# Optimization experiments

Measured on AMD Instinct MI355X. Metric: run time of the kernel, lower is better.

Reference implementation:

```python
import jax, jax.numpy as jnp
import numpy as np

DIM = 256
N_EMBED = 8192
DECAY = 0.1
COMMITMENT = 1.0
EPS = 1e-05


def setup_inputs() -> dict:
    key = jax.random.key(0)
    k1, k2, k3, k4 = jax.random.split(key, 4)
    return {
        "input": jax.random.normal(k1, (8, 1024, DIM), dtype=jnp.float32),
        "embed": jax.random.normal(k2, (DIM, N_EMBED), dtype=jnp.float32),
        "cluster_size": jax.random.uniform(k3, (N_EMBED,), dtype=jnp.float32),
        "embed_avg": jax.random.normal(k4, (DIM, N_EMBED), dtype=jnp.float32),
    }


def reference(input, embed, cluster_size, embed_avg):
    dtype = input.dtype
    flatten = input.reshape(-1, DIM)  # [N, dim]
    # squared euclidean distance to each code: [N, n_embed]
    dist = (
        jnp.sum(flatten * flatten, axis=1, keepdims=True)
        - 2.0 * (flatten @ embed)
        + jnp.sum(embed * embed, axis=0, keepdims=True)
    )
    embed_ind_flat = jnp.argmin(dist, axis=1)  # [N]
    embed_ind = embed_ind_flat.reshape(input.shape[:-1])
    quantize = jnp.take(embed.T, embed_ind, axis=0)  # [..., dim]

    # EMA codebook update (training path), via segment sums instead of dense one-hot
    bins = jax.ops.segment_sum(
        jnp.ones_like(embed_ind_flat, dtype=dtype), embed_ind_flat, num_segments=N_EMBED
    )  # one_hot.sum(0)
    embed_sum = jax.ops.segment_sum(flatten, embed_ind_flat, num_segments=N_EMBED).T  # [dim, n_embed]
    cluster_size_new = cluster_size * DECAY + (1.0 - DECAY) * bins
    embed_avg_new = embed_avg * DECAY + (1.0 - DECAY) * embed_sum
    smoothed = (cluster_size_new + EPS) / (jnp.sum(cluster_size_new) + N_EMBED * EPS)
    cs = smoothed * jnp.sum(cluster_size_new)
    embed_normalized = embed_avg_new / cs[None, :]

    commit_loss = jnp.mean((jax.lax.stop_gradient(quantize) - input) ** 2) * COMMITMENT
    quantize_st = input + jax.lax.stop_gradient(quantize - input)
    return (quantize_st, embed_ind, commit_loss, embed_normalized, cluster_size_new, embed_avg_new)
```

## Files before the change

kernel.cpp:

```cpp
#include <hip/hip_runtime.h>

typedef unsigned short u16;
typedef __attribute__((ext_vector_type(8))) short short8;
typedef __attribute__((ext_vector_type(4))) float f32x4;

#define DIM    256
#define NE     8192
#define NROWS  8192
#define DECAY  0.1f
#define EPS_F  1e-5f
#define CRANGES 16
#define CPAIRS  16
#define MQ      384u

#define OUT_Q    0
#define OUT_IND  2097152
#define OUT_LOSS 2105344
#define OUT_NORM 2105345
#define OUT_CSN  4202497
#define OUT_AVG  4210689

#define WS_CAND  65536
#define WS_ENORM 1114112
#define WS_BASEQ 1146880
#define WS_SUM   1179648
#define WS_BINS  9568256
#define WS_LOSS  9601024
#define WS_S     9601032
#define WS_XB    9601040
#define WS_ETB   13795344
#define WS_ET32  17989648
#define WS_ZLEN  (WS_XB - WS_SUM)

__device__ __forceinline__ unsigned f32_ord(float f)
{
    unsigned u = __float_as_uint(f);
    return (u & 0x80000000u) ? ~u : (u | 0x80000000u);
}
__device__ __forceinline__ u16 bf16rne(float f)
{
    unsigned u = __float_as_uint(f);
    return (u16)((u + 0x7fffu + ((u >> 16) & 1u)) >> 16);
}
__device__ __forceinline__ void gload16(const void* g, void* l)
{
    __builtin_amdgcn_global_load_lds((const __attribute__((address_space(1))) unsigned int*)g,
                                     (__attribute__((address_space(3))) unsigned int*)l, 16, 0, 0);
}

__global__ __launch_bounds__(256) void vq_cvt_x_k(const float* __restrict__ X, u16* __restrict__ Xb)
{
    const int i = blockIdx.x * 256 + threadIdx.x;
    const float4 a = ((const float4*)X)[i * 2];
    const float4 b = ((const float4*)X)[i * 2 + 1];
    short8 v;
    v[0] = (short)bf16rne(a.x); v[1] = (short)bf16rne(a.y);
    v[2] = (short)bf16rne(a.z); v[3] = (short)bf16rne(a.w);
    v[4] = (short)bf16rne(b.x); v[5] = (short)bf16rne(b.y);
    v[6] = (short)bf16rne(b.z); v[7] = (short)bf16rne(b.w);
    *(short8*)(Xb + (size_t)i * 8) = v;
}

__global__ __launch_bounds__(256) void vq_trans_e_k(const float* __restrict__ E,
                                                    float* __restrict__ ET32,
                                                    u16* __restrict__ ETb,
                                                    float* __restrict__ enorm,
                                                    float* __restrict__ baseq)
{
    __shared__ float T[64][65];
    const int t = threadIdx.x;
    const int j0 = blockIdx.x * 64;
    const int jc = t >> 2, seg = t & 3;
    const int j = j0 + jc;
    float esum = 0.f;

    for (int d0 = 0; d0 < DIM; d0 += 64) {
        if (d0) __syncthreads();
        #pragma unroll
        for (int p = 0; p < 4; ++p) {
            const int dr = p * 16 + (t >> 4);
            const float4 v = *(const float4*)(E + (size_t)(d0 + dr) * NE + j0 + (t & 15) * 4);
            T[dr][(t & 15) * 4 + 0] = v.x; T[dr][(t & 15) * 4 + 1] = v.y;
            T[dr][(t & 15) * 4 + 2] = v.z; T[dr][(t & 15) * 4 + 3] = v.w;
        }
        __syncthreads();
        float vals[16];
        #pragma unroll
        for (int i = 0; i < 16; ++i) vals[i] = T[seg * 16 + i][jc];
        float4* o32 = (float4*)(ET32 + (size_t)j * DIM + d0 + seg * 16);
        o32[0] = make_float4(vals[0], vals[1], vals[2], vals[3]);
        o32[1] = make_float4(vals[4], vals[5], vals[6], vals[7]);
        o32[2] = make_float4(vals[8], vals[9], vals[10], vals[11]);
        o32[3] = make_float4(vals[12], vals[13], vals[14], vals[15]);
        short8 b0, b1;
        #pragma unroll
        for (int i = 0; i < 8; ++i) { b0[i] = (short)bf16rne(vals[i]); b1[i] = (short)bf16rne(vals[8 + i]); }
        *(short8*)(ETb + (size_t)j * DIM + d0 + seg * 16) = b0;
        *(short8*)(ETb + (size_t)j * DIM + d0 + seg * 16 + 8) = b1;
        #pragma unroll
        for (int i = 0; i < 16; ++i) esum += vals[i] * vals[i];
    }
    esum += __shfl_xor(esum, 1, 4);
    esum += __shfl_xor(esum, 2, 4);
    if (seg == 0) {
        enorm[j] = esum;
        baseq[j] = (esum + 512.f) * 256.f;
    }
}

__global__ __launch_bounds__(256, 2) void vq_scan_k(const u16* __restrict__ Xb,
                                                    const u16* __restrict__ ETb,
                                                    const float* __restrict__ baseq,
                                                    unsigned* __restrict__ cand)
{
    __shared__ u16 Bs[2][16][512];

    const int tid = threadIdx.x;
    const int w = tid >> 6, l = tid & 63;
    const int lane16 = l & 15, g = l >> 4;
    const int rowbase = blockIdx.x * 256 + w * 64;
    const int c0 = blockIdx.y * 512;

    short8 af[4][8];
    #pragma unroll
    for (int sub = 0; sub < 4; ++sub)
        #pragma unroll
        for (int k8 = 0; k8 < 8; ++k8) {
            af[sub][k8] = *(const short8*)(Xb + (size_t)(rowbase + sub * 16 + lane16) * DIM + k8 * 32 + g * 8);
            asm volatile("" : "+a"(af[sub][k8]));
        }

    unsigned s0[16], s1[16];
    #pragma unroll
    for (int i = 0; i < 16; ++i) { s0[i] = 0xFFFFFFFFu; s1[i] = 0xFFFFFFFFu; }

    const u16* gsrc = ETb + (size_t)(c0 + lane16) * DIM + (size_t)w * 64 + g * 8;

    gload16(gsrc,                 &Bs[0][2 * w + 0][0]);
    gload16(gsrc + 32,            &Bs[0][2 * w + 1][0]);
    gload16(gsrc + 16 * DIM,      &Bs[0][8 + 2 * w + 0][0]);
    gload16(gsrc + 16 * DIM + 32, &Bs[0][8 + 2 * w + 1][0]);
    asm volatile("s_waitcnt vmcnt(0)" ::: "memory");
    __builtin_amdgcn_s_barrier();

    int buf = 0;
    #pragma unroll 1
    for (int p = 0; p < CPAIRS; ++p) {
        if (p + 1 < CPAIRS) {
            const u16* nsrc = gsrc + (size_t)(p + 1) * 32 * DIM;
            gload16(nsrc,                 &Bs[buf ^ 1][2 * w + 0][0]);
            gload16(nsrc + 32,            &Bs[buf ^ 1][2 * w + 1][0]);
            gload16(nsrc + 16 * DIM,      &Bs[buf ^ 1][8 + 2 * w + 0][0]);
            gload16(nsrc + 16 * DIM + 32, &Bs[buf ^ 1][8 + 2 * w + 1][0]);
        }
        #pragma unroll
        for (int half = 0; half < 2; ++half) {
            const int col = c0 + (p * 2 + half) * 16 + lane16;
            const float bq = baseq[col];
            f32x4 acc[4];
            #pragma unroll
            for (int sub = 0; sub < 4; ++sub) acc[sub] = {0.f, 0.f, 0.f, 0.f};
            #pragma unroll
            for (int k8 = 0; k8 < 8; ++k8) {
                const short8 bf = *(const short8*)&Bs[buf][half * 8 + k8][l * 8];
                #pragma unroll
                for (int sub = 0; sub < 4; ++sub)
                    acc[sub] = __builtin_amdgcn_mfma_f32_16x16x32_bf16(af[sub][k8], bf, acc[sub], 0, 0, 0);
            }
            #pragma unroll
            for (int sub = 0; sub < 4; ++sub)
                #pragma unroll
                for (int r = 0; r < 4; ++r) {
                    const int i = sub * 4 + r;
                    const float qf = fmaf(acc[sub][r], -512.f, bq);
                    const unsigned key = (((unsigned)qf) << 13) | (unsigned)col;
                    const unsigned t = max(s0[i], key);
                    s0[i] = min(s0[i], key);
                    s1[i] = min(s1[i], t);
                }
        }
        asm volatile("s_waitcnt vmcnt(0)" ::: "memory");
        __builtin_amdgcn_s_barrier();
        buf ^= 1;
    }

    #pragma unroll
    for (int m = 1; m < 16; m <<= 1) {
        #pragma unroll
        for (int i = 0; i < 16; ++i) {
            const unsigned o0 = __shfl_xor(s0[i], m);
            const unsigned o1 = __shfl_xor(s1[i], m);
            const unsigned t0 = min(s0[i], o0);
            const unsigned t1 = min(max(s0[i], o0), min(s1[i], o1));
            s0[i] = t0; s1[i] = t1;
        }
    }
    if (lane16 == 0) {
        #pragma unroll
        for (int i = 0; i < 16; ++i) {
            const int row = rowbase + (i >> 2) * 16 + g * 4 + (i & 3);
            cand[((size_t)row * CRANGES + blockIdx.y) * 2 + 0] = s0[i];
            cand[((size_t)row * CRANGES + blockIdx.y) * 2 + 1] = s1[i];
        }
    }
}

__global__ __launch_bounds__(256) void vq_finalize_k(const unsigned* __restrict__ cand,
                                                     const float* __restrict__ X,
                                                     const float* __restrict__ ET32,
                                                     const float* __restrict__ enorm,
                                                     float* __restrict__ out_q,
                                                     float* __restrict__ out_ind,
                                                     float* __restrict__ ws_sum,
                                                     float* __restrict__ bins,
                                                     double* __restrict__ loss)
{
    __shared__ int sj[4];
    const int tid = threadIdx.x;
    const int w = tid >> 6, l = tid & 63;
    const int row = blockIdx.x * 4 + w;

    unsigned key = 0xFFFFFFFFu;
    if (l < 32) key = cand[(size_t)row * 32 + l];
    unsigned qmin = key;
    #pragma unroll
    for (int m = 32; m; m >>= 1) qmin = min(qmin, __shfl_xor(qmin, m));
    const unsigned qthr = (qmin >> 13) + MQ;
    unsigned long long mask = __ballot((l < 32) && ((key >> 13) <= qthr));
    const float4 xv = *(const float4*)(X + (size_t)row * DIM + l * 4);
    unsigned long long best = 0xFFFFFFFFFFFFFFFFull;
    while (mask) {
        const int src = __builtin_ctzll(mask);
        mask &= mask - 1;
        const int col = (int)(__shfl(key, src) & 8191u);
        const float4 ev = *(const float4*)(ET32 + (size_t)col * DIM + l * 4);
        float s = xv.x * ev.x + xv.y * ev.y + xv.z * ev.z + xv.w * ev.w;
        #pragma unroll
        for (int m = 32; m; m >>= 1) s += __shfl_xor(s, m);
        const float d = enorm[col] - 2.f * s;
        const unsigned long long k64 = ((unsigned long long)f32_ord(d) << 32) | (unsigned)col;
        best = (k64 < best) ? k64 : best;
    }
    if (l == 0) {
        const int j = (int)(best & 8191u);
        sj[w] = j;
        out_ind[row] = (float)j;
    }
    __syncthreads();

    float lsum = 0.f;
    #pragma unroll
    for (int q = 0; q < 4; ++q) {
        const int r = blockIdx.x * 4 + q;
        const int j = sj[q];
        const float x  = X[(size_t)r * DIM + tid];
        const float qv = ET32[(size_t)j * DIM + tid];
        out_q[(size_t)r * DIM + tid] = x + (qv - x);
        const float d = qv - x;
        lsum += d * d;
        atomicAdd(&ws_sum[(size_t)j * DIM + tid], x);
        if (tid == 0) atomicAdd(&bins[j], 1.0f);
    }
    #pragma unroll
    for (int off = 32; off > 0; off >>= 1) lsum += __shfl_down(lsum, off);
    __shared__ double wred[4];
    if ((tid & 63) == 0) wred[tid >> 6] = (double)lsum;
    __syncthreads();
    if (tid == 0) atomicAdd(loss, wred[0] + wred[1] + wred[2] + wred[3]);
}

__global__ __launch_bounds__(256) void vq_csn_k(const float* __restrict__ cs,
                                                const float* __restrict__ bins,
                                                float* __restrict__ out_csn,
                                                float* __restrict__ out_loss,
                                                const double* __restrict__ loss,
                                                double* __restrict__ S)
{
    const int tid = threadIdx.x;
    const int i = blockIdx.x * 256 + tid;
    const float csn = cs[i] * DECAY + (1.0f - DECAY) * bins[i];
    out_csn[i] = csn;
    double v = (double)csn;
    #pragma unroll
    for (int off = 32; off > 0; off >>= 1) v += __shfl_down(v, off);
    __shared__ double wred[4];
    if ((tid & 63) == 0) wred[tid >> 6] = v;
    __syncthreads();
    if (tid == 0) atomicAdd(S, wred[0] + wred[1] + wred[2] + wred[3]);
    if (blockIdx.x == 0 && tid == 0) out_loss[0] = (float)(loss[0] * (1.0 / 2097152.0));
}

__global__ __launch_bounds__(256) void vq_embed_k(const float* __restrict__ EA,
                                                  const float* __restrict__ cs,
                                                  const float* __restrict__ bins,
                                                  const float* __restrict__ ws_sum,
                                                  const double* __restrict__ Sp,
                                                  float* __restrict__ out_norm,
                                                  float* __restrict__ out_avg)
{
    __shared__ float T[64][69];
    const int tid = threadIdx.x;
    const int j0 = blockIdx.x * 64;
    const int d0 = blockIdx.y * 64;
    #pragma unroll
    for (int p = 0; p < 4; ++p) {
        const int jr = (tid >> 4) + p * 16;
        const int dc = (tid & 15) * 4;
        const float4 v = *(const float4*)(ws_sum + (size_t)(j0 + jr) * DIM + d0 + dc);
        T[jr][dc + 0] = v.x; T[jr][dc + 1] = v.y; T[jr][dc + 2] = v.z; T[jr][dc + 3] = v.w;
    }
    __syncthreads();
    const double S = Sp[0];
    const float fac = (float)(S / (S + (double)NE * 1e-5));
    const int jc = tid & 63;
    const int j  = j0 + jc;
    const float csn  = cs[j] * DECAY + (1.0f - DECAY) * bins[j];
    const float cs_j = (csn + EPS_F) * fac;
    const int drb = (tid >> 6) * 16;
    #pragma unroll
    for (int p = 0; p < 16; ++p) {
        const int dr = drb + p;
        const float sum = T[jc][dr];
        const float ea  = EA[(size_t)(d0 + dr) * NE + j];
        const float ean = DECAY * ea + (1.0f - DECAY) * sum;
        out_avg[(size_t)(d0 + dr) * NE + j]  = ean;
        out_norm[(size_t)(d0 + dr) * NE + j] = ean / cs_j;
    }
}

extern "C" void kernel_launch(void* const* d_in, const int* in_sizes, int n_in,
                              void* d_out, int out_size, void* d_ws, size_t ws_size,
                              hipStream_t stream)
{
    const float* X  = (const float*)d_in[0];
    const float* E  = (const float*)d_in[1];
    const float* CS = (const float*)d_in[2];
    const float* EA = (const float*)d_in[3];
    float* out = (float*)d_out;
    char*  ws  = (char*)d_ws;

    unsigned* cand  = (unsigned*)(ws + WS_CAND);
    float*  enorm  = (float*)(ws + WS_ENORM);
    float*  baseq  = (float*)(ws + WS_BASEQ);
    float*  ws_sum = (float*)(ws + WS_SUM);
    float*  bins   = (float*)(ws + WS_BINS);
    double* loss   = (double*)(ws + WS_LOSS);
    double* S      = (double*)(ws + WS_S);
    u16*    Xb     = (u16*)(ws + WS_XB);
    u16*    ETb    = (u16*)(ws + WS_ETB);
    float*  ET32   = (float*)(ws + WS_ET32);

    hipMemsetAsync(ws + WS_SUM, 0, WS_ZLEN, stream);

    vq_cvt_x_k<<<1024, 256, 0, stream>>>(X, Xb);
    vq_trans_e_k<<<NE / 64, 256, 0, stream>>>(E, ET32, ETb, enorm, baseq);
    vq_scan_k<<<dim3(NROWS / 256, CRANGES), 256, 0, stream>>>(Xb, ETb, baseq, cand);
    vq_finalize_k<<<NROWS / 4, 256, 0, stream>>>(cand, X, ET32, enorm, out + OUT_Q, out + OUT_IND, ws_sum, bins, loss);
    vq_csn_k<<<NE / 256, 256, 0, stream>>>(CS, bins, out + OUT_CSN, out + OUT_LOSS, loss, S);
    vq_embed_k<<<dim3(NE / 64, DIM / 64), 256, 0, stream>>>(EA, CS, bins, ws_sum, S, out + OUT_NORM, out + OUT_AVG);
}
```

Measured before the change: 107.5 us.

## Merge prep kernels, fold csn into embed, widen scan tiles, add MFMA priority

Combines the X bf16 conversion and the codebook transpose into one prep kernel that also sums cluster_size. The later kernel that computed the new cluster sizes is removed. Its sum is instead derived algebraically from the cluster_size sum, since the bins always total the row count, and its output writes move into the embed kernel. This removes two launches and an atomic reduction. The scan kernel's LDS tile is doubled to stage 64 codes per iteration, halving barrier count, and s_setprio is raised around the MFMA block. The larger LDS footprint may lower occupancy.

New measurement: 103.5 us. -3.8%, faster.

```diff
diff --git a/kernel.cpp b/kernel.cpp
--- a/kernel.cpp
+++ b/kernel.cpp
@@ -10,7 +10,7 @@
 #define DECAY  0.1f
 #define EPS_F  1e-5f
 #define CRANGES 16
-#define CPAIRS  16
+#define CPH     8
 #define MQ      384u
 
 #define OUT_Q    0
@@ -26,7 +26,7 @@
 #define WS_SUM   1179648
 #define WS_BINS  9568256
 #define WS_LOSS  9601024
-#define WS_S     9601032
+#define WS_SCS   9601032
 #define WS_XB    9601040
 #define WS_ETB   13795344
 #define WS_ET32  17989648
@@ -48,63 +48,84 @@
                                      (__attribute__((address_space(3))) unsigned int*)l, 16, 0, 0);
 }
 
-__global__ __launch_bounds__(256) void vq_cvt_x_k(const float* __restrict__ X, u16* __restrict__ Xb)
-{
-    const int i = blockIdx.x * 256 + threadIdx.x;
-    const float4 a = ((const float4*)X)[i * 2];
-    const float4 b = ((const float4*)X)[i * 2 + 1];
-    short8 v;
-    v[0] = (short)bf16rne(a.x); v[1] = (short)bf16rne(a.y);
-    v[2] = (short)bf16rne(a.z); v[3] = (short)bf16rne(a.w);
-    v[4] = (short)bf16rne(b.x); v[5] = (short)bf16rne(b.y);
-    v[6] = (short)bf16rne(b.z); v[7] = (short)bf16rne(b.w);
-    *(short8*)(Xb + (size_t)i * 8) = v;
-}
-
-__global__ __launch_bounds__(256) void vq_trans_e_k(const float* __restrict__ E,
-                                                    float* __restrict__ ET32,
-                                                    u16* __restrict__ ETb,
-                                                    float* __restrict__ enorm,
-                                                    float* __restrict__ baseq)
-{
-    __shared__ float T[64][65];
+__global__ __launch_bounds__(256) void vq_prep_k(const float* __restrict__ X,
+                                                 const float* __restrict__ E,
+                                                 const float* __restrict__ CS,
+                                                 u16* __restrict__ Xb,
+                                                 float* __restrict__ ET32,
+                                                 u16* __restrict__ ETb,
+                                                 float* __restrict__ enorm,
+                                                 float* __restrict__ baseq,
+                                                 double* __restrict__ sumcs)
+{
+    const int bid = blockIdx.x;
     const int t = threadIdx.x;
-    const int j0 = blockIdx.x * 64;
-    const int jc = t >> 2, seg = t & 3;
-    const int j = j0 + jc;
-    float esum = 0.f;
-
-    for (int d0 = 0; d0 < DIM; d0 += 64) {
-        if (d0) __syncthreads();
-        #pragma unroll
-        for (int p = 0; p < 4; ++p) {
-            const int dr = p * 16 + (t >> 4);
-            const float4 v = *(const float4*)(E + (size_t)(d0 + dr) * NE + j0 + (t & 15) * 4);
-            T[dr][(t & 15) * 4 + 0] = v.x; T[dr][(t & 15) * 4 + 1] = v.y;
-            T[dr][(t & 15) * 4 + 2] = v.z; T[dr][(t & 15) * 4 + 3] = v.w;
-        }
+
+    if (bid < 128) {
+        __shared__ float T[64][65];
+        const int j0 = bid * 64;
+        const int jc = t >> 2, seg = t & 3;
+        const int j = j0 + jc;
+        float esum = 0.f;
+        for (int d0 = 0; d0 < DIM; d0 += 64) {
+            if (d0) __syncthreads();
+            #pragma unroll
+            for (int p = 0; p < 4; ++p) {
+                const int dr = p * 16 + (t >> 4);
+                const float4 v = *(const float4*)(E + (size_t)(d0 + dr) * NE + j0 + (t & 15) * 4);
+                T[dr][(t & 15) * 4 + 0] = v.x; T[dr][(t & 15) * 4 + 1] = v.y;
+                T[dr][(t & 15) * 4 + 2] = v.z; T[dr][(t & 15) * 4 + 3] = v.w;
+            }
+            __syncthreads();
+            float vals[16];
+            #pragma unroll
+            for (int i = 0; i < 16; ++i) vals[i] = T[seg * 16 + i][jc];
+            float4* o32 = (float4*)(ET32 + (size_t)j * DIM + d0 + seg * 16);
+            o32[0] = make_float4(vals[0], vals[1], vals[2], vals[3]);
+            o32[1] = make_float4(vals[4], vals[5], vals[6], vals[7]);
+            o32[2] = make_float4(vals[8], vals[9], vals[10], vals[11]);
+            o32[3] = make_float4(vals[12], vals[13], vals[14], vals[15]);
+            short8 b0, b1;
+            #pragma unroll
+            for (int i = 0; i < 8; ++i) { b0[i] = (short)bf16rne(vals[i]); b1[i] = (short)bf16rne(vals[8 + i]); }
+            *(short8*)(ETb + (size_t)j * DIM + d0 + seg * 16) = b0;
+            *(short8*)(ETb + (size_t)j * DIM + d0 + seg * 16 + 8) = b1;
+            #pragma unroll
+            for (int i = 0; i < 16; ++i) esum += vals[i] * vals[i];
+        }
+        esum += __shfl_xor(esum, 1, 4);
+        esum += __shfl_xor(esum, 2, 4);
+        if (seg == 0) {
+            enorm[j] = esum;
+            baseq[j] = (esum + 512.f) * 256.f;
+        }
+    } else if (bid < 256) {
+        const int chunk = bid - 128;
+        #pragma unroll
+        for (int it = 0; it < 8; ++it) {
+            const int gi = chunk * 2048 + it * 256 + t;
+            const float4 a = ((const float4*)X)[gi * 2];
+            const float4 b = ((const float4*)X)[gi * 2 + 1];
+            short8 v;
+            v[0] = (short)bf16rne(a.x); v[1] = (short)bf16rne(a.y);
+            v[2] = (short)bf16rne(a.z); v[3] = (short)bf16rne(a.w);
+            v[4] = (short)bf16rne(b.x); v[5] = (short)bf16rne(b.y);
+            v[6] = (short)bf16rne(b.z); v[7] = (short)bf16rne(b.w);
+            *(short8*)(Xb + (size_t)gi * 8) = v;
+        }
+    } else {
+        double s = 0.0;
+        #pragma unroll
+        for (int it = 0; it < 8; ++it) {
+            const float4 v = ((const float4*)CS)[it * 256 + t];
+            s += (double)v.x + (double)v.y + (double)v.z + (double)v.w;
+        }
+        #pragma unroll
+        for (int off = 32; off > 0; off >>= 1) s += __shfl_down(s, off);
+        __shared__ double wred[4];
+        if ((t & 63) == 0) wred[t >> 6] = s;
         __syncthreads();
-        float vals[16];
-        #pragma unroll
-        for (int i = 0; i < 16; ++i) vals[i] = T[seg * 16 + i][jc];
-        float4* o32 = (float4*)(ET32 + (size_t)j * DIM + d0 + seg * 16);
-        o32[0] = make_float4(vals[0], vals[1], vals[2], vals[3]);
-        o32[1] = make_float4(vals[4], vals[5], vals[6], vals[7]);
-        o32[2] = make_float4(vals[8], vals[9], vals[10], vals[11]);
-        o32[3] = make_float4(vals[12], vals[13], vals[14], vals[15]);
-        short8 b0, b1;
-        #pragma unroll
-        for (int i = 0; i < 8; ++i) { b0[i] = (short)bf16rne(vals[i]); b1[i] = (short)bf16rne(vals[8 + i]); }
-        *(short8*)(ETb + (size_t)j * DIM + d0 + seg * 16) = b0;
-        *(short8*)(ETb + (size_t)j * DIM + d0 + seg * 16 + 8) = b1;
-        #pragma unroll
-        for (int i = 0; i < 16; ++i) esum += vals[i] * vals[i];
-    }
-    esum += __shfl_xor(esum, 1, 4);
-    esum += __shfl_xor(esum, 2, 4);
-    if (seg == 0) {
-        enorm[j] = esum;
-        baseq[j] = (esum + 512.f) * 256.f;
+        if (t == 0) sumcs[0] = wred[0] + wred[1] + wred[2] + wred[3];
     }
 }
 
@@ -113,7 +134,7 @@
                                                     const float* __restrict__ baseq,
                                                     unsigned* __restrict__ cand)
 {
-    __shared__ u16 Bs[2][16][512];
+    __shared__ u16 Bs[2][32][512];
 
     const int tid = threadIdx.x;
     const int w = tid >> 6, l = tid & 63;
@@ -136,30 +157,33 @@
 
     const u16* gsrc = ETb + (size_t)(c0 + lane16) * DIM + (size_t)w * 64 + g * 8;
 
-    gload16(gsrc,                 &Bs[0][2 * w + 0][0]);
-    gload16(gsrc + 32,            &Bs[0][2 * w + 1][0]);
-    gload16(gsrc + 16 * DIM,      &Bs[0][8 + 2 * w + 0][0]);
-    gload16(gsrc + 16 * DIM + 32, &Bs[0][8 + 2 * w + 1][0]);
+    #pragma unroll
+    for (int tt = 0; tt < 4; ++tt) {
+        gload16(gsrc + (size_t)tt * 16 * DIM,      &Bs[0][tt * 8 + 2 * w + 0][0]);
+        gload16(gsrc + (size_t)tt * 16 * DIM + 32, &Bs[0][tt * 8 + 2 * w + 1][0]);
+    }
     asm volatile("s_waitcnt vmcnt(0)" ::: "memory");
     __builtin_amdgcn_s_barrier();
 
     int buf = 0;
     #pragma unroll 1
-    for (int p = 0; p < CPAIRS; ++p) {
-        if (p + 1 < CPAIRS) {
-            const u16* nsrc = gsrc + (size_t)(p + 1) * 32 * DIM;
-            gload16(nsrc,                 &Bs[buf ^ 1][2 * w + 0][0]);
-            gload16(nsrc + 32,            &Bs[buf ^ 1][2 * w + 1][0]);
-            gload16(nsrc + 16 * DIM,      &Bs[buf ^ 1][8 + 2 * w + 0][0]);
-            gload16(nsrc + 16 * DIM + 32, &Bs[buf ^ 1][8 + 2 * w + 1][0]);
-        }
-        #pragma unroll
-        for (int half = 0; half < 2; ++half) {
-            const int col = c0 + (p * 2 + half) * 16 + lane16;
+    for (int p = 0; p < CPH; ++p) {
+        if (p + 1 < CPH) {
+            const u16* nsrc = gsrc + (size_t)(p + 1) * 64 * DIM;
+            #pragma unroll
+            for (int tt = 0; tt < 4; ++tt) {
+                gload16(nsrc + (size_t)tt * 16 * DIM,      &Bs[buf ^ 1][tt * 8 + 2 * w + 0][0]);
+                gload16(nsrc + (size_t)tt * 16 * DIM + 32, &Bs[buf ^ 1][tt * 8 + 2 * w + 1][0]);
+            }
+        }
+        #pragma unroll
+        for (int half = 0; half < 4; ++half) {
+            const int col = c0 + (p * 4 + half) * 16 + lane16;
             const float bq = baseq[col];
             f32x4 acc[4];
             #pragma unroll
             for (int sub = 0; sub < 4; ++sub) acc[sub] = {0.f, 0.f, 0.f, 0.f};
+            __builtin_amdgcn_s_setprio(1);
             #pragma unroll
             for (int k8 = 0; k8 < 8; ++k8) {
                 const short8 bf = *(const short8*)&Bs[buf][half * 8 + k8][l * 8];
@@ -167,6 +191,7 @@
                 for (int sub = 0; sub < 4; ++sub)
                     acc[sub] = __builtin_amdgcn_mfma_f32_16x16x32_bf16(af[sub][k8], bf, acc[sub], 0, 0, 0);
             }
+            __builtin_amdgcn_s_setprio(0);
             #pragma unroll
             for (int sub = 0; sub < 4; ++sub)
                 #pragma unroll
@@ -174,9 +199,9 @@
                     const int i = sub * 4 + r;
                     const float qf = fmaf(acc[sub][r], -512.f, bq);
                     const unsigned key = (((unsigned)qf) << 13) | (unsigned)col;
-                    const unsigned t = max(s0[i], key);
+                    const unsigned tt = max(s0[i], key);
                     s0[i] = min(s0[i], key);
-                    s1[i] = min(s1[i], t);
+                    s1[i] = min(s1[i], tt);
                 }
         }
         asm volatile("s_waitcnt vmcnt(0)" ::: "memory");
@@ -269,34 +294,16 @@
     if (tid == 0) atomicAdd(loss, wred[0] + wred[1] + wred[2] + wred[3]);
 }
 
-__global__ __launch_bounds__(256) void vq_csn_k(const float* __restrict__ cs,
-                                                const float* __restrict__ bins,
-                                                float* __restrict__ out_csn,
-                                                float* __restrict__ out_loss,
-                                                const double* __restrict__ loss,
-                                                double* __restrict__ S)
-{
-    const int tid = threadIdx.x;
-    const int i = blockIdx.x * 256 + tid;
-    const float csn = cs[i] * DECAY + (1.0f - DECAY) * bins[i];
-    out_csn[i] = csn;
-    double v = (double)csn;
-    #pragma unroll
-    for (int off = 32; off > 0; off >>= 1) v += __shfl_down(v, off);
-    __shared__ double wred[4];
-    if ((tid & 63) == 0) wred[tid >> 6] = v;
-    __syncthreads();
-    if (tid == 0) atomicAdd(S, wred[0] + wred[1] + wred[2] + wred[3]);
-    if (blockIdx.x == 0 && tid == 0) out_loss[0] = (float)(loss[0] * (1.0 / 2097152.0));
-}
-
 __global__ __launch_bounds__(256) void vq_embed_k(const float* __restrict__ EA,
                                                   const float* __restrict__ cs,
                                                   const float* __restrict__ bins,
                                                   const float* __restrict__ ws_sum,
-                                                  const double* __restrict__ Sp,
+                                                  const double* __restrict__ sumcs,
+                                                  const double* __restrict__ loss,
                                                   float* __restrict__ out_norm,
-                                                  float* __restrict__ out_avg)
+                                                  float* __restrict__ out_avg,
+                                                  float* __restrict__ out_csn,
+                                                  float* __restrict__ out_loss)
 {
     __shared__ float T[64][69];
     const int tid = threadIdx.x;
@@ -310,12 +317,14 @@
         T[jr][dc + 0] = v.x; T[jr][dc + 1] = v.y; T[jr][dc + 2] = v.z; T[jr][dc + 3] = v.w;
     }
     __syncthreads();
-    const double S = Sp[0];
+    const double S = (double)DECAY * sumcs[0] + (double)(1.0f - DECAY) * (double)NROWS;
     const float fac = (float)(S / (S + (double)NE * 1e-5));
     const int jc = tid & 63;
     const int j  = j0 + jc;
     const float csn  = cs[j] * DECAY + (1.0f - DECAY) * bins[j];
     const float cs_j = (csn + EPS_F) * fac;
+    if (blockIdx.y == 0 && tid < 64) out_csn[j0 + tid] = cs[j0 + tid] * DECAY + (1.0f - DECAY) * bins[j0 + tid];
+    if (blockIdx.y == 0 && blockIdx.x == 0 && tid == 0) out_loss[0] = (float)(loss[0] * (1.0 / 2097152.0));
     const int drb = (tid >> 6) * 16;
     #pragma unroll
     for (int p = 0; p < 16; ++p) {
@@ -345,17 +354,16 @@
     float*  ws_sum = (float*)(ws + WS_SUM);
     float*  bins   = (float*)(ws + WS_BINS);
     double* loss   = (double*)(ws + WS_LOSS);
-    double* S      = (double*)(ws + WS_S);
+    double* sumcs  = (double*)(ws + WS_SCS);
     u16*    Xb     = (u16*)(ws + WS_XB);
     u16*    ETb    = (u16*)(ws + WS_ETB);
     float*  ET32   = (float*)(ws + WS_ET32);
 
     hipMemsetAsync(ws + WS_SUM, 0, WS_ZLEN, stream);
 
-    vq_cvt_x_k<<<1024, 256, 0, stream>>>(X, Xb);
-    vq_trans_e_k<<<NE / 64, 256, 0, stream>>>(E, ET32, ETb, enorm, baseq);
+    vq_prep_k<<<257, 256, 0, stream>>>(X, E, CS, Xb, ET32, ETb, enorm, baseq, sumcs);
     vq_scan_k<<<dim3(NROWS / 256, CRANGES), 256, 0, stream>>>(Xb, ETb, baseq, cand);
     vq_finalize_k<<<NROWS / 4, 256, 0, stream>>>(cand, X, ET32, enorm, out + OUT_Q, out + OUT_IND, ws_sum, bins, loss);
-    vq_csn_k<<<NE / 256, 256, 0, stream>>>(CS, bins, out + OUT_CSN, out + OUT_LOSS, loss, S);
-    vq_embed_k<<<dim3(NE / 64, DIM / 64), 256, 0, stream>>>(EA, CS, bins, ws_sum, S, out + OUT_NORM, out + OUT_AVG);
-}
+    vq_embed_k<<<dim3(NE / 64, DIM / 64), 256, 0, stream>>>(EA, CS, bins, ws_sum, sumcs, loss,
+                                                            out + OUT_NORM, out + OUT_AVG, out + OUT_CSN, out + OUT_LOSS);
+}
```
